# Optimization experiments

Hardware: AMD Instinct MI355X
Metric: run time of the kernel (lower is better)

## Reference

```python
import jax, jax.numpy as jnp
import numpy as np

B, N, C, K = 2, 2048, 384, 20
EPS = 1e-5
SLOPE = 0.2


def _bn(h, g, b, m, v):
    # inference-mode batchnorm over channel (last) axis
    return (h - m) * (g * jax.lax.rsqrt(v + EPS)) + b


def _edge_conv(x, W, g, b, m, v):
    # x: [B, N, C] point features. Standard DGCNN EdgeConv.
    sq = jnp.sum(x * x, axis=-1)                              # [B, N]
    inner = jnp.einsum('bnc,bmc->bnm', x, x)                  # [B, N, N]
    neg_dist = 2.0 * inner - sq[:, :, None] - sq[:, None, :]  # -||xi-xj||^2
    _, idx = jax.lax.top_k(neg_dist, K)                       # [B, N, K] nearest (incl. self)
    neigh = jax.vmap(lambda xb, ib: xb[ib])(x, idx)           # [B, N, K, C]
    center = x[:, :, None, :]                                  # [B, N, 1, C]
    edge = jnp.concatenate(
        [neigh - center, jnp.broadcast_to(center, neigh.shape)], axis=-1)  # [B,N,K,2C]
    h = jnp.einsum('bnkc,oc->bnko', edge, W)                  # 1x1 conv2d, bias=False
    h = jax.nn.leaky_relu(_bn(h, g, b, m, v), negative_slope=SLOPE)
    return jnp.max(h, axis=2)                                  # max over K -> [B, N, C_out]


def setup_inputs() -> dict:
    key = jax.random.key(0)
    ks = jax.random.split(key, 12)
    d = {}
    d['x'] = jax.random.normal(ks[0], (B, C, N), jnp.float32)
    d['pos'] = jax.random.normal(ks[1], (B, 3, N), jnp.float32)
    for i, s in enumerate(['1', '2', '3']):
        d['We' + s] = jax.random.normal(ks[2 + i], (C, 2 * C), jnp.float32) * 0.05
        d['g' + s] = 1.0 + 0.1 * jax.random.normal(ks[5 + i], (C,), jnp.float32)
        d['b' + s] = 0.1 * jax.random.normal(ks[8 + i], (C,), jnp.float32)
        d['m' + s] = jnp.zeros((C,), jnp.float32)
        d['v' + s] = jnp.ones((C,), jnp.float32)
    d['Wp'] = jax.random.normal(ks[11], (C, 3 * C), jnp.float32) * 0.05
    d['gp'] = jnp.ones((C,), jnp.float32)
    d['bp'] = jnp.zeros((C,), jnp.float32)
    d['mp'] = jnp.zeros((C,), jnp.float32)
    d['vp'] = jnp.ones((C,), jnp.float32)
    return d


def reference(x, pos, We1, g1, b1, m1, v1, We2, g2, b2, m2, v2,
              We3, g3, b3, m3, v3, Wp, gp, bp, mp, vp):
    xb = jnp.transpose(x, (0, 2, 1))                # [B, N, C]
    x1 = _edge_conv(xb, We1, g1, b1, m1, v1)
    x2 = _edge_conv(x1, We2, g2, b2, m2, v2)
    x3 = _edge_conv(x2, We3, g3, b3, m3, v3)
    h = jnp.concatenate([x1, x2, x3], axis=-1)      # [B, N, 3C]
    h = jnp.einsum('bnc,oc->bno', h, Wp)            # 1x1 conv1d, bias=False
    h = jax.nn.leaky_relu(_bn(h, gp, bp, mp, vp), negative_slope=SLOPE)
    return jnp.max(h, axis=1, keepdims=True)        # adaptive_max_pool1d(1).transpose -> [B, 1, C]
```

## Files before the change

kernel.cpp:

```cpp
#include <hip/hip_runtime.h>
#include <hip/hip_bf16.h>
#include <cstdint>
#include <cstddef>

#define B_ 2
#define N_ 2048
#define C_ 384
#define K_ 20
#define EPS_ 1e-5f
#define SLOPE_ 0.2f

typedef __attribute__((ext_vector_type(8))) short short8;
typedef __attribute__((ext_vector_type(4))) short short4v;
typedef __attribute__((ext_vector_type(4))) float floatx4;

#define MFMA(a, b, c) __builtin_amdgcn_mfma_f32_16x16x32_bf16((a), (b), (c), 0, 0, 0)

__device__ __forceinline__ unsigned fmap(float f) {
  unsigned u = __float_as_uint(f);
  return (u & 0x80000000u) ? ~u : (u | 0x80000000u);
}
__device__ __forceinline__ float funmap(unsigned u) {
  unsigned bits = (u & 0x80000000u) ? (u ^ 0x80000000u) : ~u;
  return __uint_as_float(bits);
}
__device__ __forceinline__ short f2b(float f) {
  __hip_bfloat16 h = __float2bfloat16(f);
  unsigned short u;
  __builtin_memcpy(&u, &h, 2);
  return (short)u;
}
__device__ __forceinline__ float b2f(short s) {
  unsigned u = ((unsigned)(unsigned short)s) << 16;
  return __uint_as_float(u);
}

__device__ __forceinline__ void stage16(const short* g, int ld, short* dst, int lane) {
  const short* src = g + (size_t)(lane & 15) * ld + ((lane >> 4) << 3);
  __builtin_amdgcn_global_load_lds(
      (const __attribute__((address_space(1))) void*)src,
      (__attribute__((address_space(3))) void*)dst, 16, 0, 0);
}

__device__ __forceinline__ void gemm128(const short* AH, const short* AL, int ldA,
                                        const short* BH, const short* BL, int ldB,
                                        short (*sst)[4096], int tid,
                                        floatx4 acc[4][4]) {
  int lane = tid & 63, w = tid >> 6;
  int wr = w >> 1, wc = w & 1;
  for (int kc = 0; kc < C_; kc += 32) {
    __syncthreads();
#pragma unroll
    for (int ss = 0; ss < 2; ss++) {
      int s = w * 2 + ss;
      int ro = s * 16;
      stage16(AH + (size_t)ro * ldA + kc, ldA, &sst[0][s * 512], lane);
      stage16(AL + (size_t)ro * ldA + kc, ldA, &sst[1][s * 512], lane);
      stage16(BH + (size_t)ro * ldB + kc, ldB, &sst[2][s * 512], lane);
      stage16(BL + (size_t)ro * ldB + kc, ldB, &sst[3][s * 512], lane);
    }
    __syncthreads();
    short8 ah[4], al[4], bh[4], bl[4];
#pragma unroll
    for (int m = 0; m < 4; m++) {
      ah[m] = *(const short8*)&sst[0][(wr * 4 + m) * 512 + lane * 8];
      al[m] = *(const short8*)&sst[1][(wr * 4 + m) * 512 + lane * 8];
      bh[m] = *(const short8*)&sst[2][(wc * 4 + m) * 512 + lane * 8];
      bl[m] = *(const short8*)&sst[3][(wc * 4 + m) * 512 + lane * 8];
    }
#pragma unroll
    for (int m = 0; m < 4; m++)
#pragma unroll
      for (int n = 0; n < 4; n++) {
        acc[m][n] = MFMA(ah[m], bh[n], acc[m][n]);
        acc[m][n] = MFMA(ah[m], bl[n], acc[m][n]);
        acc[m][n] = MFMA(al[m], bh[n], acc[m][n]);
      }
  }
}

__global__ __launch_bounds__(256) void k_prep(
    const float* __restrict__ x,
    const float* __restrict__ We0, const float* __restrict__ g0, const float* __restrict__ b0,
    const float* __restrict__ m0, const float* __restrict__ v0,
    const float* __restrict__ We1, const float* __restrict__ g1, const float* __restrict__ b1,
    const float* __restrict__ m1, const float* __restrict__ v1,
    const float* __restrict__ We2, const float* __restrict__ g2, const float* __restrict__ b2,
    const float* __restrict__ m2, const float* __restrict__ v2,
    const float* __restrict__ Wp, const float* __restrict__ gp, const float* __restrict__ bp,
    const float* __restrict__ mp, const float* __restrict__ vp,
    short* __restrict__ H0, short* __restrict__ L0,
    short* __restrict__ WbfH, short* __restrict__ WbfL,
    short* __restrict__ WpH, short* __restrict__ WpL,
    float* __restrict__ bz, float* __restrict__ bz2,
    unsigned* __restrict__ stage) {
  __shared__ float tile[32][33];
  int bx = blockIdx.x;
  if (bx < 3456) {
    int l = bx / 1152;
    int t = (bx % 1152) * 256 + threadIdx.x;
    const float* We = (l == 0) ? We0 : (l == 1) ? We1 : We2;
    const float* g  = (l == 0) ? g0  : (l == 1) ? g1  : g2;
    const float* bb = (l == 0) ? b0  : (l == 1) ? b1  : b2;
    const float* m  = (l == 0) ? m0  : (l == 1) ? m1  : m2;
    const float* v  = (l == 0) ? v0  : (l == 1) ? v1  : v2;
    short* WH = WbfH + (size_t)l * 2 * C_ * C_;
    short* WL = WbfL + (size_t)l * 2 * C_ * C_;
    float* bzl = bz + (size_t)l * 2 * C_;
    int o2 = t / C_, c = t % C_;
    int o = (o2 < C_) ? o2 : (o2 - C_);
    float sc = g[o] * rsqrtf(v[o] + EPS_);
    float w = (o2 < C_) ? sc * We[(size_t)o * 2 * C_ + c]
                        : sc * (We[(size_t)o * 2 * C_ + C_ + c] - We[(size_t)o * 2 * C_ + c]);
    short hb = f2b(w);
    WH[t] = hb;
    WL[t] = f2b(w - b2f(hb));
    if (t < 2 * C_)
      bzl[t] = (t < C_) ? 0.f
                        : (bb[t - C_] - m[t - C_] * (g[t - C_] * rsqrtf(v[t - C_] + EPS_)));
  } else if (bx < 5184) {
    int t = (bx - 3456) * 256 + threadIdx.x;
    int o = t / (3 * C_);
    float sc = gp[o] * rsqrtf(vp[o] + EPS_);
    float w = sc * Wp[t];
    short hb = f2b(w);
    WpH[t] = hb;
    WpL[t] = f2b(w - b2f(hb));
    if (t < C_) {
      float s2 = gp[t] * rsqrtf(vp[t] + EPS_);
      bz2[t] = bp[t] - mp[t] * s2;
    }
  } else if (bx < 5187) {
    int t = (bx - 5184) * 256 + threadIdx.x;
    if (t < B_ * C_) stage[t] = 0x007FFFFFu;
  } else {
    int i = bx - 5187;
    int bn = i % 64, bc = (i / 64) % 12, b = i / 768;
    int tx = threadIdx.x & 31, ty = threadIdx.x >> 5;
    const float* src = x + ((size_t)b * C_ + bc * 32) * N_ + bn * 32;
#pragma unroll
    for (int j = 0; j < 32; j += 8)
      tile[ty + j][tx] = src[(size_t)(ty + j) * N_ + tx];
    __syncthreads();
#pragma unroll
    for (int j = 0; j < 32; j += 8) {
      float val = tile[tx][ty + j];
      short hb = f2b(val);
      short lb = f2b(val - b2f(hb));
      size_t off = ((size_t)b * N_ + bn * 32 + ty + j) * C_ + bc * 32 + tx;
      H0[off] = hb;
      L0[off] = lb;
    }
  }
}

__global__ __launch_bounds__(256) void k_rowsq(const short* __restrict__ H,
                                               const short* __restrict__ L,
                                               float* __restrict__ sq) {
  int row  = blockIdx.x * 4 + (threadIdx.x >> 6);
  int lane = threadIdx.x & 63;
  const short* ph = H + (size_t)row * C_;
  const short* pl = L + (size_t)row * C_;
  float v = 0.f;
  if (lane < C_ / 8) {
    short8 h8 = *(const short8*)(ph + lane * 8);
    short8 l8 = *(const short8*)(pl + lane * 8);
#pragma unroll
    for (int j = 0; j < 8; j++) {
      float t = b2f(h8[j]) + b2f(l8[j]);
      v += t * t;
    }
  }
#pragma unroll
  for (int off = 32; off; off >>= 1) v += __shfl_xor(v, off, 64);
  if (lane == 0) sq[row] = v;
}

__global__ __launch_bounds__(256) void k_gramyz(const short* __restrict__ H,
                                                const short* __restrict__ L,
                                                int ldh, int coff,
                                                const float* __restrict__ sq,
                                                float* __restrict__ Gm,
                                                const short* __restrict__ WH,
                                                const short* __restrict__ WL,
                                                const float* __restrict__ bz,
                                                float* __restrict__ YZ) {
  __shared__ __align__(16) short sst[4][4096];
  int bx = blockIdx.x;
  int tid = threadIdx.x, lane = tid & 63, w = tid >> 6;
  int wr = w >> 1, wc = w & 1;
  int fr = lane & 15, r0 = (lane >> 4) << 2;
  floatx4 acc[4][4] = {};

  if (bx < 136 * B_) {
    int b = bx / 136, t = bx % 136;
    int p = (int)((sqrtf(8.f * t + 1.f) - 1.f) * 0.5f);
    while ((p + 1) * (p + 2) / 2 <= t) p++;
    while (p * (p + 1) / 2 > t) p--;
    int q = t - p * (p + 1) / 2;
    int bi = q, bj = p;

    const short* Hb = H + (size_t)b * N_ * ldh + coff;
    const short* Lb = L + (size_t)b * N_ * ldh + coff;
    gemm128(Hb + (size_t)(bi * 128) * ldh, Lb + (size_t)(bi * 128) * ldh, ldh,
            Hb + (size_t)(bj * 128) * ldh, Lb + (size_t)(bj * 128) * ldh, ldh,
            sst, tid, acc);

    const float* sqb = sq + (size_t)b * N_;
    float* gbase = Gm + (size_t)b * N_ * N_;
    int rbase = bi * 128 + wr * 64;
    int cbase = bj * 128 + wc * 64;
#pragma unroll
    for (int n = 0; n < 4; n++) {
      int col = cbase + n * 16 + fr;
      float sqB = sqb[col];
#pragma unroll
      for (int m = 0; m < 4; m++)
#pragma unroll
        for (int i = 0; i < 4; i++)
          gbase[(size_t)(rbase + m * 16 + r0 + i) * N_ + col] = 2.f * acc[m][n][i] - sqB;
    }
    if (bi != bj) {
#pragma unroll
      for (int m = 0; m < 4; m++) {
        int mc0 = rbase + m * 16 + r0;
        float4 sqA = *(const float4*)(sqb + mc0);
        float sqs[4] = {sqA.x, sqA.y, sqA.z, sqA.w};
#pragma unroll
        for (int n = 0; n < 4; n++) {
          int mrow = cbase + n * 16 + fr;
          float4 mv = make_float4(2.f * acc[m][n][0] - sqs[0], 2.f * acc[m][n][1] - sqs[1],
                                  2.f * acc[m][n][2] - sqs[2], 2.f * acc[m][n][3] - sqs[3]);
          *(float4*)(gbase + (size_t)mrow * N_ + mc0) = mv;
        }
      }
    }
  } else {
    int i = bx - 136 * B_;
    int bi = i & 15, bj = (i >> 4) % 6, b = i / (16 * 6);
    const short* Hb = H + (size_t)b * N_ * ldh + coff;
    const short* Lb = L + (size_t)b * N_ * ldh + coff;
    gemm128(Hb + (size_t)(bi * 128) * ldh, Lb + (size_t)(bi * 128) * ldh, ldh,
            WH + (size_t)(bj * 128) * C_, WL + (size_t)(bj * 128) * C_, C_,
            sst, tid, acc);
    int rbase = bi * 128 + wr * 64;
    int cbase = bj * 128 + wc * 64;
#pragma unroll
    for (int n = 0; n < 4; n++) {
      int gcol = cbase + n * 16 + fr;
      float bzv = bz[gcol];
#pragma unroll
      for (int m = 0; m < 4; m++)
#pragma unroll
        for (int i2 = 0; i2 < 4; i2++)
          YZ[((size_t)b * N_ + rbase + m * 16 + r0 + i2) * (2 * C_) + gcol] =
              acc[m][n][i2] + bzv;
    }
  }
}

__device__ __forceinline__ void tk_insert(float v, int j, bool valid,
                                          float& t0, float& t1, float& t2, float& t3,
                                          int& j0, int& j1, int& j2, int& j3) {
  bool c0 = valid && (v > t0);
  bool c1 = valid && (v > t1);
  bool c2 = valid && (v > t2);
  bool c3 = valid && (v > t3);
  t3 = c2 ? t2 : (c3 ? v : t3);  j3 = c2 ? j2 : (c3 ? j : j3);
  t2 = c1 ? t1 : (c2 ? v : t2);  j2 = c1 ? j1 : (c2 ? j : j2);
  t1 = c0 ? t0 : (c1 ? v : t1);  j1 = c0 ? j0 : (c1 ? j : j1);
  t0 = c0 ? v : t0;              j0 = c0 ? j : j0;
}

__device__ __forceinline__ void tk_refill(const float* va, int lane,
                                          float lastV, int lastJ,
                                          float& t0, float& t1, float& t2, float& t3,
                                          int& j0, int& j1, int& j2, int& j3) {
  t0 = t1 = t2 = t3 = -INFINITY;
  j0 = j1 = j2 = j3 = 0x7FFFFFFF;
#pragma unroll
  for (int s = 0; s < 32; s++) {
    int j = (s >> 2) * 256 + lane * 4 + (s & 3);
    float v = va[s];
    bool valid = (v < lastV) || (v == lastV && j > lastJ);
    tk_insert(v, j, valid, t0, t1, t2, t3, j0, j1, j2, j3);
  }
}

__global__ __launch_bounds__(256) void k_topk(const float* __restrict__ Gm,
                                              int* __restrict__ idx) {
  int lane = threadIdx.x & 63, wv = threadIdx.x >> 6;
  int n = blockIdx.x * 4 + wv, b = blockIdx.y;
  const float4* grow = (const float4*)(Gm + ((size_t)b * N_ + n) * N_);
  float va[32];
#pragma unroll
  for (int q = 0; q < 8; q++) {
    float4 t4 = grow[q * 64 + lane];
    va[q * 4 + 0] = t4.x; va[q * 4 + 1] = t4.y;
    va[q * 4 + 2] = t4.z; va[q * 4 + 3] = t4.w;
  }
  float t0, t1, t2, t3;
  int j0, j1, j2, j3;
  tk_refill(va, lane, INFINITY, -1, t0, t1, t2, t3, j0, j1, j2, j3);
  float lastV = INFINITY;
  int lastJ = -1;
  int mysel = 0;
  for (int it = 0; it < K_; it++) {
    float gv = t0;
    int gj = j0;
#pragma unroll
    for (int off = 32; off; off >>= 1) {
      float v2 = __shfl_xor(gv, off, 64);
      int i2 = __shfl_xor(gj, off, 64);
      if (v2 > gv || (v2 == gv && i2 < gj)) { gv = v2; gj = i2; }
    }
    if (lane == it) mysel = gj;
    if (j0 == gj) {
      lastV = t0; lastJ = j0;
      t0 = t1; j0 = j1;
      t1 = t2; j1 = j2;
      t2 = t3; j2 = j3;
      t3 = -INFINITY; j3 = 0x7FFFFFFF;
    }
    if (t0 == -INFINITY && it < K_ - 1)
      tk_refill(va, lane, lastV, lastJ, t0, t1, t2, t3, j0, j1, j2, j3);
  }
  if (lane < K_) idx[((size_t)b * N_ + n) * K_ + lane] = mysel;
}

__global__ __launch_bounds__(384) void k_combine(const float* __restrict__ YZ,
                                                 const int* __restrict__ idx,
                                                 short* __restrict__ Hout,
                                                 short* __restrict__ Lout, int cofo,
                                                 float* __restrict__ sq) {
  __shared__ int sidx[4][K_];
  __shared__ float sred[384];
  int n0 = blockIdx.x * 4, b = blockIdx.y, t = threadIdx.x;
  if (t < 4 * K_) {
    int qq = t / K_, r = t % K_;
    sidx[qq][r] = idx[((size_t)b * N_ + n0 + qq) * K_ + r];
  }
  __syncthreads();
  int ro = t / 96, oc = (t % 96) * 4;
  int n = n0 + ro;
  const float* baseYZ = YZ + (size_t)b * N_ * (2 * C_);
  float4 z = *(const float4*)(baseYZ + (size_t)n * (2 * C_) + C_ + oc);
  float4 mx = make_float4(-INFINITY, -INFINITY, -INFINITY, -INFINITY);
#pragma unroll
  for (int k = 0; k < K_; k++) {
    float4 y = *(const float4*)(baseYZ + (size_t)sidx[ro][k] * (2 * C_) + oc);
    mx.x = fmaxf(mx.x, y.x + z.x);
    mx.y = fmaxf(mx.y, y.y + z.y);
    mx.z = fmaxf(mx.z, y.z + z.z);
    mx.w = fmaxf(mx.w, y.w + z.w);
  }
  float vv[4] = {mx.x, mx.y, mx.z, mx.w};
  short4v hs, ls;
  float ssum = 0.f;
#pragma unroll
  for (int j = 0; j < 4; j++) {
    float s = vv[j];
    s = s > 0.f ? s : SLOPE_ * s;
    short hb = f2b(s);
    short lb = f2b(s - b2f(hb));
    hs[j] = hb;
    ls[j] = lb;
    float tv = b2f(hb) + b2f(lb);
    ssum += tv * tv;
  }
  size_t off = ((size_t)b * N_ + n) * (3 * C_) + cofo + oc;
  *(short4v*)(Hout + off) = hs;
  *(short4v*)(Lout + off) = ls;
  sred[t] = ssum;
  __syncthreads();
  if (t < 4) {
    float s = 0.f;
    for (int u = 0; u < 96; u++) s += sred[t * 96 + u];
    sq[(size_t)b * N_ + n0 + t] = s;
  }
}

__global__ __launch_bounds__(256) void k_finpart(const short* __restrict__ Hcat,
                                                 const short* __restrict__ Lcat,
                                                 const short* __restrict__ WpH,
                                                 const short* __restrict__ WpL,
                                                 float* __restrict__ Pf) {
  __shared__ __align__(16) short sst[4][4096];
  int bi = blockIdx.x, bj = blockIdx.y;
  int b = blockIdx.z / 3, ks = blockIdx.z % 3;
  int K0 = ks * C_;
  int tid = threadIdx.x, lane = tid & 63, w = tid >> 6;
  int wr = w >> 1, wc = w & 1;
  int fr = lane & 15, r0 = (lane >> 4) << 2;
  const short* Hb = Hcat + (size_t)b * N_ * (3 * C_) + K0;
  const short* Lb = Lcat + (size_t)b * N_ * (3 * C_) + K0;
  floatx4 acc[4][4] = {};
  gemm128(Hb + (size_t)(bi * 128) * (3 * C_), Lb + (size_t)(bi * 128) * (3 * C_), 3 * C_,
          WpH + (size_t)(bj * 128) * (3 * C_) + K0, WpL + (size_t)(bj * 128) * (3 * C_) + K0,
          3 * C_, sst, tid, acc);
  float* Pb = Pf + ((size_t)ks * B_ + b) * N_ * C_;
  int rbase = bi * 128 + wr * 64;
  int cbase = bj * 128 + wc * 64;
#pragma unroll
  for (int n = 0; n < 4; n++) {
    int gcol = cbase + n * 16 + fr;
#pragma unroll
    for (int m = 0; m < 4; m++)
#pragma unroll
      for (int i = 0; i < 4; i++)
        Pb[(size_t)(rbase + m * 16 + r0 + i) * C_ + gcol] = acc[m][n][i];
  }
}

__global__ __launch_bounds__(384) void k_finred(const float* __restrict__ Pf,
                                                const float* __restrict__ bz2,
                                                unsigned* __restrict__ stage) {
  int nc = blockIdx.x, b = blockIdx.y, o = threadIdx.x;
  const size_t spl = (size_t)B_ * N_ * C_;
  float bzv = bz2[o];
  float vmax = -INFINITY;
  for (int nn = 0; nn < 16; nn++) {
    size_t base = ((size_t)b * N_ + nc * 16 + nn) * C_ + o;
    float y = Pf[base] + Pf[base + spl] + Pf[base + 2 * spl] + bzv;
    y = y > 0.f ? y : SLOPE_ * y;
    vmax = fmaxf(vmax, y);
  }
  atomicMax(stage + (size_t)b * C_ + o, fmap(vmax));
}

__global__ void k_unmap(const unsigned* __restrict__ stage, float* __restrict__ out) {
  int t = blockIdx.x * 256 + threadIdx.x;
  if (t < B_ * C_) out[t] = funmap(stage[t]);
}

extern "C" void kernel_launch(void* const* d_in, const int* in_sizes, int n_in,
                              void* d_out, int out_size, void* d_ws, size_t ws_size,
                              hipStream_t stream) {
  const float* x   = (const float*)d_in[0];
  const float* We[3] = {(const float*)d_in[2], (const float*)d_in[7], (const float*)d_in[12]};
  const float* g[3]  = {(const float*)d_in[3], (const float*)d_in[8], (const float*)d_in[13]};
  const float* bb[3] = {(const float*)d_in[4], (const float*)d_in[9], (const float*)d_in[14]};
  const float* m[3]  = {(const float*)d_in[5], (const float*)d_in[10], (const float*)d_in[15]};
  const float* v[3]  = {(const float*)d_in[6], (const float*)d_in[11], (const float*)d_in[16]};
  const float* Wp = (const float*)d_in[17];
  const float* gp = (const float*)d_in[18];
  const float* bp = (const float*)d_in[19];
  const float* mp = (const float*)d_in[20];
  const float* vp = (const float*)d_in[21];
  float* out = (float*)d_out;

  float* Gm = (float*)d_ws;
  float* Pf = Gm;
  float* YZ = Gm + (size_t)B_ * N_ * N_;
  float* sq = YZ + (size_t)B_ * N_ * 2 * C_;
  int* idx = (int*)(sq + (size_t)B_ * N_);
  short* Hcat = (short*)(idx + (size_t)B_ * N_ * K_);
  short* Lcat = Hcat + (size_t)B_ * N_ * 3 * C_;
  short* H0   = Lcat + (size_t)B_ * N_ * 3 * C_;
  short* L0   = H0 + (size_t)B_ * N_ * C_;
  short* WbfH = L0 + (size_t)B_ * N_ * C_;
  short* WbfL = WbfH + (size_t)3 * 2 * C_ * C_;
  short* WpH  = WbfL + (size_t)3 * 2 * C_ * C_;
  short* WpL  = WpH + (size_t)C_ * 3 * C_;
  float* bz   = (float*)(WpL + (size_t)C_ * 3 * C_);
  float* bz2  = bz + 3 * 2 * C_;
  unsigned* stage = (unsigned*)(bz2 + C_);

  k_prep<<<dim3(5187 + 1536), 256, 0, stream>>>(
      x, We[0], g[0], bb[0], m[0], v[0], We[1], g[1], bb[1], m[1], v[1],
      We[2], g[2], bb[2], m[2], v[2], Wp, gp, bp, mp, vp,
      H0, L0, WbfH, WbfL, WpH, WpL, bz, bz2, stage);
  k_rowsq<<<dim3(B_ * N_ / 4), 256, 0, stream>>>(H0, L0, sq);

  for (int l = 0; l < 3; l++) {
    const short* Hin = (l == 0) ? H0 : Hcat;
    const short* Lin = (l == 0) ? L0 : Lcat;
    int ldh  = (l == 0) ? C_ : 3 * C_;
    int coff = (l == 0) ? 0 : (l - 1) * C_;

    k_gramyz<<<dim3(136 * B_ + 16 * 6 * B_), 256, 0, stream>>>(
        Hin, Lin, ldh, coff, sq, Gm,
        WbfH + (size_t)l * 2 * C_ * C_, WbfL + (size_t)l * 2 * C_ * C_,
        bz + (size_t)l * 2 * C_, YZ);
    k_topk<<<dim3(N_ / 4, B_), 256, 0, stream>>>(Gm, idx);
    k_combine<<<dim3(N_ / 4, B_), 384, 0, stream>>>(YZ, idx, Hcat, Lcat, l * C_, sq);
  }

  k_finpart<<<dim3(N_ / 128, C_ / 128, B_ * 3), 256, 0, stream>>>(Hcat, Lcat, WpH, WpL, Pf);
  k_finred<<<dim3(N_ / 16, B_), 384, 0, stream>>>(Pf, bz2, stage);
  k_unmap<<<dim3((B_ * C_ + 255) / 256), 256, 0, stream>>>(stage, out);
}
```

Before: 243.5 us.

## Fuse top-k selection with neighbor combine and remap gram blocks per XCD

Merges the top-k kernel and the gather/max combine kernel into one wave-per-point kernel. Selected indices now pass between lanes by shuffle instead of going through a global idx buffer, and the sum of squares is reduced with wave shuffles instead of shared memory. The per-lane candidate list shrinks from 4 to 2 entries, which cuts registers but forces refills more often. Block IDs in k_gramyz are also remapped so that consecutive logical tiles land on the same XCD for better L2 locality. The trade-off is that each wave now does the combine work with less parallelism than the separate 384-thread combine kernel had.

```diff
diff --git a/kernel.cpp b/kernel.cpp
--- a/kernel.cpp
+++ b/kernel.cpp
@@ -186,7 +186,11 @@
                                                 const float* __restrict__ bz,
                                                 float* __restrict__ YZ) {
   __shared__ __align__(16) short sst[4][4096];
-  int bx = blockIdx.x;
+  int orig = blockIdx.x, nwg = gridDim.x;
+  int xcd = orig & 7, loc = orig >> 3;
+  int qq_ = nwg >> 3, rr_ = nwg & 7;
+  int bx = (xcd < rr_) ? (xcd * (qq_ + 1) + loc) : (rr_ * (qq_ + 1) + (xcd - rr_) * qq_ + loc);
+
   int tid = threadIdx.x, lane = tid & 63, w = tid >> 6;
   int wr = w >> 1, wc = w & 1;
   int fr = lane & 15, r0 = (lane >> 4) << 2;
@@ -259,38 +263,36 @@
   }
 }
 
-__device__ __forceinline__ void tk_insert(float v, int j, bool valid,
-                                          float& t0, float& t1, float& t2, float& t3,
-                                          int& j0, int& j1, int& j2, int& j3) {
+__device__ __forceinline__ void tk_insert2(float v, int j, bool valid,
+                                           float& t0, float& t1, int& j0, int& j1) {
   bool c0 = valid && (v > t0);
   bool c1 = valid && (v > t1);
-  bool c2 = valid && (v > t2);
-  bool c3 = valid && (v > t3);
-  t3 = c2 ? t2 : (c3 ? v : t3);  j3 = c2 ? j2 : (c3 ? j : j3);
-  t2 = c1 ? t1 : (c2 ? v : t2);  j2 = c1 ? j1 : (c2 ? j : j2);
   t1 = c0 ? t0 : (c1 ? v : t1);  j1 = c0 ? j0 : (c1 ? j : j1);
   t0 = c0 ? v : t0;              j0 = c0 ? j : j0;
 }
 
-__device__ __forceinline__ void tk_refill(const float* va, int lane,
-                                          float lastV, int lastJ,
-                                          float& t0, float& t1, float& t2, float& t3,
-                                          int& j0, int& j1, int& j2, int& j3) {
-  t0 = t1 = t2 = t3 = -INFINITY;
-  j0 = j1 = j2 = j3 = 0x7FFFFFFF;
+__device__ __forceinline__ void tk_refill2(const float* va, int lane,
+                                           float lastV, int lastJ,
+                                           float& t0, float& t1, int& j0, int& j1) {
+  t0 = t1 = -INFINITY;
+  j0 = j1 = 0x7FFFFFFF;
 #pragma unroll
   for (int s = 0; s < 32; s++) {
     int j = (s >> 2) * 256 + lane * 4 + (s & 3);
     float v = va[s];
     bool valid = (v < lastV) || (v == lastV && j > lastJ);
-    tk_insert(v, j, valid, t0, t1, t2, t3, j0, j1, j2, j3);
-  }
-}
-
-__global__ __launch_bounds__(256) void k_topk(const float* __restrict__ Gm,
-                                              int* __restrict__ idx) {
-  int lane = threadIdx.x & 63, wv = threadIdx.x >> 6;
-  int n = blockIdx.x * 4 + wv, b = blockIdx.y;
+    tk_insert2(v, j, valid, t0, t1, j0, j1);
+  }
+}
+
+__global__ __launch_bounds__(256) void k_select(const float* __restrict__ Gm,
+                                                const float* __restrict__ YZ,
+                                                short* __restrict__ Hout,
+                                                short* __restrict__ Lout, int cofo,
+                                                float* __restrict__ sq) {
+  int lane = threadIdx.x & 63, w = threadIdx.x >> 6;
+  int n = blockIdx.x * 4 + w, b = blockIdx.y;
+
   const float4* grow = (const float4*)(Gm + ((size_t)b * N_ + n) * N_);
   float va[32];
 #pragma unroll
@@ -299,9 +301,13 @@
     va[q * 4 + 0] = t4.x; va[q * 4 + 1] = t4.y;
     va[q * 4 + 2] = t4.z; va[q * 4 + 3] = t4.w;
   }
-  float t0, t1, t2, t3;
-  int j0, j1, j2, j3;
-  tk_refill(va, lane, INFINITY, -1, t0, t1, t2, t3, j0, j1, j2, j3);
+  float t0 = -INFINITY, t1 = -INFINITY;
+  int j0 = 0x7FFFFFFF, j1 = 0x7FFFFFFF;
+#pragma unroll
+  for (int s = 0; s < 32; s++) {
+    int j = (s >> 2) * 256 + lane * 4 + (s & 3);
+    tk_insert2(va[s], j, true, t0, t1, j0, j1);
+  }
   float lastV = INFINITY;
   int lastJ = -1;
   int mysel = 0;
@@ -318,66 +324,49 @@
     if (j0 == gj) {
       lastV = t0; lastJ = j0;
       t0 = t1; j0 = j1;
-      t1 = t2; j1 = j2;
-      t2 = t3; j2 = j3;
-      t3 = -INFINITY; j3 = 0x7FFFFFFF;
+      t1 = -INFINITY; j1 = 0x7FFFFFFF;
     }
     if (t0 == -INFINITY && it < K_ - 1)
-      tk_refill(va, lane, lastV, lastJ, t0, t1, t2, t3, j0, j1, j2, j3);
-  }
-  if (lane < K_) idx[((size_t)b * N_ + n) * K_ + lane] = mysel;
-}
-
-__global__ __launch_bounds__(384) void k_combine(const float* __restrict__ YZ,
-                                                 const int* __restrict__ idx,
-                                                 short* __restrict__ Hout,
-                                                 short* __restrict__ Lout, int cofo,
-                                                 float* __restrict__ sq) {
-  __shared__ int sidx[4][K_];
-  __shared__ float sred[384];
-  int n0 = blockIdx.x * 4, b = blockIdx.y, t = threadIdx.x;
-  if (t < 4 * K_) {
-    int qq = t / K_, r = t % K_;
-    sidx[qq][r] = idx[((size_t)b * N_ + n0 + qq) * K_ + r];
-  }
-  __syncthreads();
-  int ro = t / 96, oc = (t % 96) * 4;
-  int n = n0 + ro;
+      tk_refill2(va, lane, lastV, lastJ, t0, t1, j0, j1);
+  }
+  int jreg[K_];
+#pragma unroll
+  for (int k = 0; k < K_; k++) jreg[k] = __shfl(mysel, k, 64);
+
   const float* baseYZ = YZ + (size_t)b * N_ * (2 * C_);
-  float4 z = *(const float4*)(baseYZ + (size_t)n * (2 * C_) + C_ + oc);
-  float4 mx = make_float4(-INFINITY, -INFINITY, -INFINITY, -INFINITY);
-#pragma unroll
-  for (int k = 0; k < K_; k++) {
-    float4 y = *(const float4*)(baseYZ + (size_t)sidx[ro][k] * (2 * C_) + oc);
-    mx.x = fmaxf(mx.x, y.x + z.x);
-    mx.y = fmaxf(mx.y, y.y + z.y);
-    mx.z = fmaxf(mx.z, y.z + z.z);
-    mx.w = fmaxf(mx.w, y.w + z.w);
-  }
-  float vv[4] = {mx.x, mx.y, mx.z, mx.w};
-  short4v hs, ls;
   float ssum = 0.f;
-#pragma unroll
-  for (int j = 0; j < 4; j++) {
-    float s = vv[j];
-    s = s > 0.f ? s : SLOPE_ * s;
-    short hb = f2b(s);
-    short lb = f2b(s - b2f(hb));
-    hs[j] = hb;
-    ls[j] = lb;
-    float tv = b2f(hb) + b2f(lb);
-    ssum += tv * tv;
-  }
-  size_t off = ((size_t)b * N_ + n) * (3 * C_) + cofo + oc;
-  *(short4v*)(Hout + off) = hs;
-  *(short4v*)(Lout + off) = ls;
-  sred[t] = ssum;
-  __syncthreads();
-  if (t < 4) {
-    float s = 0.f;
-    for (int u = 0; u < 96; u++) s += sred[t * 96 + u];
-    sq[(size_t)b * N_ + n0 + t] = s;
-  }
+  for (int cc = lane; cc < 96; cc += 64) {
+    int oc = cc * 4;
+    float4 z = *(const float4*)(baseYZ + (size_t)n * (2 * C_) + C_ + oc);
+    float4 mx = make_float4(-INFINITY, -INFINITY, -INFINITY, -INFINITY);
+#pragma unroll
+    for (int k = 0; k < K_; k++) {
+      float4 y = *(const float4*)(baseYZ + (size_t)jreg[k] * (2 * C_) + oc);
+      mx.x = fmaxf(mx.x, y.x + z.x);
+      mx.y = fmaxf(mx.y, y.y + z.y);
+      mx.z = fmaxf(mx.z, y.z + z.z);
+      mx.w = fmaxf(mx.w, y.w + z.w);
+    }
+    float vv[4] = {mx.x, mx.y, mx.z, mx.w};
+    short4v hs, ls;
+#pragma unroll
+    for (int j = 0; j < 4; j++) {
+      float s = vv[j];
+      s = s > 0.f ? s : SLOPE_ * s;
+      short hb = f2b(s);
+      short lb = f2b(s - b2f(hb));
+      hs[j] = hb;
+      ls[j] = lb;
+      float tv = b2f(hb) + b2f(lb);
+      ssum += tv * tv;
+    }
+    size_t off = ((size_t)b * N_ + n) * (3 * C_) + cofo + oc;
+    *(short4v*)(Hout + off) = hs;
+    *(short4v*)(Lout + off) = ls;
+  }
+#pragma unroll
+  for (int off = 32; off; off >>= 1) ssum += __shfl_xor(ssum, off, 64);
+  if (lane == 0) sq[(size_t)b * N_ + n] = ssum;
 }
 
 __global__ __launch_bounds__(256) void k_finpart(const short* __restrict__ Hcat,
@@ -453,8 +442,7 @@
   float* Pf = Gm;
   float* YZ = Gm + (size_t)B_ * N_ * N_;
   float* sq = YZ + (size_t)B_ * N_ * 2 * C_;
-  int* idx = (int*)(sq + (size_t)B_ * N_);
-  short* Hcat = (short*)(idx + (size_t)B_ * N_ * K_);
+  short* Hcat = (short*)(sq + (size_t)B_ * N_);
   short* Lcat = Hcat + (size_t)B_ * N_ * 3 * C_;
   short* H0   = Lcat + (size_t)B_ * N_ * 3 * C_;
   short* L0   = H0 + (size_t)B_ * N_ * C_;
@@ -482,8 +470,7 @@
         Hin, Lin, ldh, coff, sq, Gm,
         WbfH + (size_t)l * 2 * C_ * C_, WbfL + (size_t)l * 2 * C_ * C_,
         bz + (size_t)l * 2 * C_, YZ);
-    k_topk<<<dim3(N_ / 4, B_), 256, 0, stream>>>(Gm, idx);
-    k_combine<<<dim3(N_ / 4, B_), 384, 0, stream>>>(YZ, idx, Hcat, Lcat, l * C_, sq);
+    k_select<<<dim3(N_ / 4, B_), 256, 0, stream>>>(Gm, YZ, Hcat, Lcat, l * C_, sq);
   }
 
   k_finpart<<<dim3(N_ / 128, C_ / 128, B_ * 3), 256, 0, stream>>>(Hcat, Lcat, WpH, WpL, Pf);
```

New measurement: 261.3 us. 1.07x slower.
